# Optimization experiments

Measured on AMD Instinct MI355X. Metric: run time of the kernel, lower is better.

## Reference

```python
import jax, jax.numpy as jnp
import numpy as np

B, T, D, H = 4, 2048, 1024, 16
DH = D // H  # head dim = 64
FLOAT_MIN = jnp.finfo(jnp.float32).min


def setup_inputs() -> dict:
    key = jax.random.key(0)
    k1, k2, k3 = jax.random.split(key, 3)
    scale = 1.0 / np.sqrt(D)
    return {
        "x": jax.random.normal(k1, (B, T, D), dtype=jnp.float32),
        "W_qkv": jax.random.normal(k2, (D, 3 * D), dtype=jnp.float32) * scale,
        "b_qkv": jnp.zeros((3 * D,), dtype=jnp.float32),
        "W_out": jax.random.normal(k3, (D, D), dtype=jnp.float32) * scale,
        "b_out": jnp.zeros((D,), dtype=jnp.float32),
        "mask": jnp.ones((B, T, T), dtype=jnp.float32),
    }


def _split_heads(t):
    # [B, T, D] -> [B, H, T, DH]
    b, s, _ = t.shape
    return t.reshape(b, s, H, DH).transpose(0, 2, 1, 3)


def reference(x, W_qkv, b_qkv, W_out, b_out, mask):
    # fused QKV projection (Conv1D kernel-size 1 == per-position dense)
    qkv = jnp.einsum("btd,de->bte", x, W_qkv) + b_qkv
    q, k, v = jnp.split(qkv, 3, axis=-1)
    q = _split_heads(q) * (DH ** -0.5)  # [B, H, T, DH]
    k = _split_heads(k)
    v = _split_heads(v)
    # scores [B, H, Tq, Tk]
    dot = jnp.einsum("bhqd,bhkd->bhqk", q, k)
    m = mask[:, None, :, :]  # expand over heads
    dot = dot * m + (1.0 - m) * FLOAT_MIN
    attn = jax.nn.softmax(dot, axis=-1)
    ctx = jnp.einsum("bhqk,bhkd->bhqd", attn, v)  # [B, H, T, DH]
    combined = ctx.transpose(0, 2, 1, 3).reshape(x.shape[0], x.shape[1], D)
    out = jnp.einsum("btd,de->bte", combined, W_out) + b_out
    return out
```

## Files before the change

kernel.cpp:

```cpp
#include <hip/hip_runtime.h>

typedef short bf16x8 __attribute__((ext_vector_type(8)));
typedef float f32x4 __attribute__((ext_vector_type(4)));
typedef float f32x16 __attribute__((ext_vector_type(16)));
typedef unsigned short u16x8 __attribute__((ext_vector_type(8)));

#define DEVI __device__ __forceinline__

static constexpr int T_ = 2048;

DEVI unsigned short f2bf(float f) {
  unsigned int x = __builtin_bit_cast(unsigned int, f);
  x += 0x7fffu + ((x >> 16) & 1u);
  return (unsigned short)(x >> 16);
}

DEVI unsigned int cvtpk(float lo, float hi2) {
  unsigned int r;
  asm("v_cvt_pk_bf16_f32 %0, %1, %2" : "=v"(r) : "v"(lo), "v"(hi2));
  return r;
}

DEVI float exp2_raw(float x) {
  float r;
  asm("v_exp_f32 %0, %1" : "=v"(r) : "v"(x));
  return r;
}

DEVI int swz23(int r) {
  const int d = ((r >> 2) ^ (r >> 3)) & 1;
  return r ^ (d << 2) ^ (d << 3);
}

DEVI bf16x8 mkfrag(unsigned a, unsigned b, unsigned c, unsigned d) {
  union { unsigned u[4]; bf16x8 v; } x;
  x.u[0] = a; x.u[1] = b; x.u[2] = c; x.u[3] = d;
  return x.v;
}

DEVI void gl2lds16(const void* g, const void* l) {
  __builtin_amdgcn_global_load_lds(
      (const __attribute__((address_space(1))) void*)g,
      (__attribute__((address_space(3))) void*)l, 16, 0, 0);
}

__global__ __launch_bounds__(256) void k_cvt_bf16(const float* __restrict__ in,
                                                  unsigned short* __restrict__ out) {
  size_t i = ((size_t)blockIdx.x * 256 + threadIdx.x) * 8;
  float4 a = *(const float4*)(in + i);
  float4 b = *(const float4*)(in + i + 4);
  u16x8 o;
  o[0] = f2bf(a.x); o[1] = f2bf(a.y); o[2] = f2bf(a.z); o[3] = f2bf(a.w);
  o[4] = f2bf(b.x); o[5] = f2bf(b.y); o[6] = f2bf(b.z); o[7] = f2bf(b.w);
  *(u16x8*)(out + i) = o;
}

__global__ __launch_bounds__(256) void k_mask_scan(const uint4* __restrict__ m,
                                                   unsigned int* __restrict__ flag) {
  const unsigned int ONE = 0x3f800000u;
  size_t i0 = ((size_t)blockIdx.x * 256 + threadIdx.x) * 8;
  bool ok = true;
#pragma unroll
  for (int i = 0; i < 8; ++i) {
    uint4 v = m[i0 + i];
    ok &= (v.x == ONE) & (v.y == ONE) & (v.z == ONE) & (v.w == ONE);
  }
  if (!ok) atomicAnd(flag, 0u);
}

template <int R, int C>
__global__ __launch_bounds__(256) void k_transpose_cvt(const float* __restrict__ in,
                                                       unsigned short* __restrict__ out) {
  __shared__ unsigned short t[64][65];
  const int c0 = blockIdx.x * 64, r0 = blockIdx.y * 64;
  const int cc = threadIdx.x & 63, r4 = threadIdx.x >> 6;
#pragma unroll
  for (int i = 0; i < 16; ++i) {
    int rr = i * 4 + r4;
    t[rr][cc] = f2bf(in[(size_t)(r0 + rr) * C + c0 + cc]);
  }
  __syncthreads();
#pragma unroll
  for (int i = 0; i < 16; ++i) {
    int rr = i * 4 + r4;
    out[(size_t)(c0 + rr) * R + r0 + cc] = t[cc][rr];
  }
}

__global__ __launch_bounds__(256) void k_transpose_v(const unsigned short* __restrict__ V,
                                                     unsigned short* __restrict__ Vt) {
  __shared__ unsigned short t[64][65];
  const int t0 = blockIdx.x * 64;
  const size_t bh = blockIdx.y;
  const unsigned short* src = V + (bh * T_ + t0) * 64;
  unsigned short* dst = Vt + bh * 64 * T_ + t0;
  const int cc = threadIdx.x & 63, r4 = threadIdx.x >> 6;
#pragma unroll
  for (int i = 0; i < 16; ++i) {
    int rr = i * 4 + r4;
    t[rr][cc] = src[(size_t)rr * 64 + cc];
  }
  __syncthreads();
#pragma unroll
  for (int i = 0; i < 16; ++i) {
    int rr = i * 4 + r4;
    dst[(size_t)rr * T_ + cc] = t[cc][rr];
  }
}

template <int EPI>
__global__ __launch_bounds__(256, 3) void k_gemm(
    const unsigned short* __restrict__ A, const unsigned short* __restrict__ Bt,
    const float* __restrict__ bias,
    unsigned short* __restrict__ qo, unsigned short* __restrict__ ko2,
    unsigned short* __restrict__ vo, float* __restrict__ fo) {
  __shared__ unsigned short As[2][128 * 32];
  __shared__ unsigned short Bs[2][128 * 32];
  const int tid = threadIdx.x;
  const int lane = tid & 63, w = tid >> 6;
  const int wr = w >> 1, wc = w & 1;
  const int g = lane >> 4, c0 = lane & 15;
  const int m0 = blockIdx.y * 128, n0 = blockIdx.x * 128;

  f32x4 acc[4][4] = {};

  const int s0 = tid, s1 = tid + 256;
  const int ar0 = s0 >> 2, ac0 = (s0 & 3) ^ ((ar0 >> 1) & 3);
  const int ar1 = s1 >> 2, ac1 = (s1 & 3) ^ ((ar1 >> 1) & 3);
  const int ldsb0 = w * 512, ldsb1 = w * 512 + 2048;

  const unsigned short* Ar0 = A + (size_t)(m0 + ar0) * 1024 + ac0 * 8;
  const unsigned short* Ar1 = A + (size_t)(m0 + ar1) * 1024 + ac1 * 8;
  const unsigned short* Br0 = Bt + (size_t)(n0 + ar0) * 1024 + ac0 * 8;
  const unsigned short* Br1 = Bt + (size_t)(n0 + ar1) * 1024 + ac1 * 8;

  auto stage = [&](int buf, int kt) {
    const int ke = kt * 32;
    gl2lds16(Ar0 + ke, &As[buf][ldsb0]);
    gl2lds16(Ar1 + ke, &As[buf][ldsb1]);
    gl2lds16(Br0 + ke, &Bs[buf][ldsb0]);
    gl2lds16(Br1 + ke, &Bs[buf][ldsb1]);
  };

  stage(0, 0);
  __syncthreads();
  int cur = 0;
  for (int kt = 0; kt < 32; ++kt) {
    if (kt + 1 < 32) stage(cur ^ 1, kt + 1);
    bf16x8 af[4], bfv[4];
#pragma unroll
    for (int mf = 0; mf < 4; ++mf) {
      int row = wr * 64 + mf * 16 + c0;
      int ch = g ^ ((row >> 1) & 3);
      af[mf] = *(const bf16x8*)&As[cur][row * 32 + ch * 8];
    }
#pragma unroll
    for (int nf = 0; nf < 4; ++nf) {
      int row = wc * 64 + nf * 16 + c0;
      int ch = g ^ ((row >> 1) & 3);
      bfv[nf] = *(const bf16x8*)&Bs[cur][row * 32 + ch * 8];
    }
    __builtin_amdgcn_s_setprio(1);
#pragma unroll
    for (int mf = 0; mf < 4; ++mf)
#pragma unroll
      for (int nf = 0; nf < 4; ++nf)
        acc[mf][nf] = __builtin_amdgcn_mfma_f32_16x16x32_bf16(af[mf], bfv[nf], acc[mf][nf], 0, 0, 0);
    __builtin_amdgcn_s_setprio(0);
    __syncthreads();
    cur ^= 1;
  }

#pragma unroll
  for (int mf = 0; mf < 4; ++mf) {
#pragma unroll
    for (int nf = 0; nf < 4; ++nf) {
      const int n = n0 + wc * 64 + nf * 16 + c0;
      const float bv = bias[n];
#pragma unroll
      for (int r = 0; r < 4; ++r) {
        const int m = m0 + wr * 64 + mf * 16 + g * 4 + r;
        float v = acc[mf][nf][r] + bv;
        if constexpr (EPI == 0) {
          const int sel = n >> 10, hd = n & 1023;
          const int h = hd >> 6, d = hd & 63;
          const int b = m >> 11, t = m & 2047;
          const size_t off = ((size_t)((b * 16 + h) * 2048 + t)) * 64 + d;
          if (sel == 0)       qo[off] = f2bf(v * 0.125f);
          else if (sel == 1)  ko2[off] = f2bf(v);
          else                vo[off] = f2bf(v);
        } else {
          fo[(size_t)m * 1024 + n] = v;
        }
      }
    }
  }
}

__global__ __launch_bounds__(256, 4) void k_attn(
    const unsigned short* __restrict__ Q, const unsigned short* __restrict__ Kg_,
    const unsigned short* __restrict__ Vt, const float* __restrict__ mask,
    const unsigned int* __restrict__ maskflag,
    unsigned short* __restrict__ ctx) {
  __shared__ unsigned short Ks[2][64 * 64];
  __shared__ unsigned short Vs[2][64 * 64];
  const int tid = threadIdx.x, lane = tid & 63, w = tid >> 6;
  const int q = lane & 31, hi = lane >> 5;

  const int flat = blockIdx.x + 16 * blockIdx.y + 256 * blockIdx.z;
  const int work = (flat & 7) * 128 + (flat >> 3);
  const int qb = work & 15;
  const int bh_i = work >> 4;
  const int h = bh_i & 15, b = bh_i >> 4;
  const int t0 = qb * 128;
  const size_t bh = (size_t)bh_i;

  const unsigned short* Qg = Q + (bh * 2048 + t0 + w * 32 + q) * 64;
  const unsigned short* Kg = Kg_ + bh * 2048 * 64;
  const unsigned short* Vg = Vt + bh * 64 * 2048;
  const float* Mg = mask + (size_t)b * 2048 * 2048;
  const bool allones = (*maskflag != 0u);

  bf16x8 qf[4];
#pragma unroll
  for (int kd = 0; kd < 4; ++kd)
    qf[kd] = *(const bf16x8*)(Qg + kd * 16 + hi * 8);

  f32x16 ot[2] = {};
  float mrun = -__builtin_inff(), lrun = 0.f;

  const int s0 = tid, s1 = tid + 256;
  const int kr0 = s0 >> 3, kc0 = (s0 & 7) ^ (kr0 & 7);
  const int kr1 = s1 >> 3, kc1 = (s1 & 7) ^ (kr1 & 7);
  const int kp0 = swz23(kr0), kp1 = swz23(kr1);
  const int ldsb0 = w * 512, ldsb1 = w * 512 + 2048;

  auto stageKV = [&](int buf, int kt) {
    gl2lds16(Kg + (size_t)(kt * 64 + kp0) * 64 + kc0 * 8, &Ks[buf][ldsb0]);
    gl2lds16(Kg + (size_t)(kt * 64 + kp1) * 64 + kc1 * 8, &Ks[buf][ldsb1]);
    gl2lds16(Vg + (size_t)kr0 * 2048 + kt * 64 + kc0 * 8, &Vs[buf][ldsb0]);
    gl2lds16(Vg + (size_t)kr1 * 2048 + kt * 64 + kc1 * 8, &Vs[buf][ldsb1]);
  };

  stageKV(0, 0);
  __syncthreads();
  int cur = 0;
  const float MINF = -3.402823466e38f;
  const float L2E = 1.4426950408889634f;

  for (int kt = 0; kt < 32; ++kt) {
    if (kt + 1 < 32) stageKV(cur ^ 1, kt + 1);

    f32x16 st[2] = {};
#pragma unroll
    for (int mt2 = 0; mt2 < 2; ++mt2) {
      __builtin_amdgcn_s_setprio(1);
#pragma unroll
      for (int kd = 0; kd < 4; ++kd) {
        const int row = mt2 * 32 + q;
        const int ch = (2 * kd + hi) ^ (row & 7);
        bf16x8 kf = *(const bf16x8*)&Ks[cur][row * 64 + ch * 8];
        st[mt2] = __builtin_amdgcn_mfma_f32_32x32x16_bf16(kf, qf[kd], st[mt2], 0, 0, 0);
      }
      __builtin_amdgcn_s_setprio(0);
    }

    if (!allones) {
      const int qg = t0 + w * 32 + q;
#pragma unroll
      for (int mt2 = 0; mt2 < 2; ++mt2)
#pragma unroll
        for (int r = 0; r < 16; ++r) {
          const int kg = kt * 64 + mt2 * 32 +
                         (r & 3) + 4 * ((r >> 2) & 1) + 8 * hi + 16 * (r >> 3);
          const float mv = Mg[(size_t)qg * 2048 + kg];
          st[mt2][r] = st[mt2][r] * mv + (1.f - mv) * MINF;
        }
    }

    float g4[8];
#pragma unroll
    for (int i = 0; i < 4; ++i) {
      g4[i]     = fmaxf(fmaxf(fmaxf(st[0][4 * i], st[0][4 * i + 1]), st[0][4 * i + 2]), st[0][4 * i + 3]);
      g4[i + 4] = fmaxf(fmaxf(fmaxf(st[1][4 * i], st[1][4 * i + 1]), st[1][4 * i + 2]), st[1][4 * i + 3]);
    }
    float r1 = fmaxf(fmaxf(g4[0], g4[1]), g4[2]);
    float r2 = fmaxf(fmaxf(g4[3], g4[4]), g4[5]);
    float r3 = fmaxf(fmaxf(g4[6], g4[7]), r1);
    float tmax = fmaxf(r2, r3);
    tmax = fmaxf(tmax, __shfl_xor(tmax, 32));
    const bool defer = (__all(tmax <= mrun + 8.f) != 0);
    float alpha = 1.f;
    if (!defer) {
      const float mnew = fmaxf(mrun, tmax);
      alpha = exp2_raw((mrun - mnew) * L2E);
      mrun = mnew;
    }
    const float mL2 = mrun * L2E;
#pragma unroll
    for (int mt2 = 0; mt2 < 2; ++mt2)
#pragma unroll
      for (int i = 0; i < 16; ++i)
        st[mt2][i] = exp2_raw(st[mt2][i] * L2E - mL2);
    float s8[8];
#pragma unroll
    for (int i = 0; i < 8; ++i)
      s8[i] = (st[0][i] + st[0][i + 8]) + (st[1][i] + st[1][i + 8]);
    float s4a = s8[0] + s8[4], s4b = s8[1] + s8[5];
    float s4c = s8[2] + s8[6], s4d = s8[3] + s8[7];
    float ps = (s4a + s4b) + (s4c + s4d);
    ps += __shfl_xor(ps, 32);
    lrun = lrun * alpha + ps;
    if (!defer) {
#pragma unroll
      for (int dt = 0; dt < 2; ++dt)
#pragma unroll
        for (int i = 0; i < 16; ++i) ot[dt][i] *= alpha;
    }

    bf16x8 pf[4];
#pragma unroll
    for (int mt2 = 0; mt2 < 2; ++mt2) {
      unsigned int pw[8];
#pragma unroll
      for (int i = 0; i < 8; ++i) pw[i] = cvtpk(st[mt2][2 * i], st[mt2][2 * i + 1]);
      pf[2 * mt2]     = mkfrag(pw[0], pw[1], pw[2], pw[3]);
      pf[2 * mt2 + 1] = mkfrag(pw[4], pw[5], pw[6], pw[7]);
    }

#pragma unroll
    for (int dt = 0; dt < 2; ++dt) {
      __builtin_amdgcn_s_setprio(1);
#pragma unroll
      for (int kt2 = 0; kt2 < 4; ++kt2) {
        const int row = dt * 32 + q;
        const int ch = (2 * kt2 + hi) ^ (row & 7);
        bf16x8 vf = *(const bf16x8*)&Vs[cur][row * 64 + ch * 8];
        ot[dt] = __builtin_amdgcn_mfma_f32_32x32x16_bf16(vf, pf[kt2], ot[dt], 0, 0, 0);
      }
      __builtin_amdgcn_s_setprio(0);
    }

    __syncthreads();
    cur ^= 1;
  }

  const int qg = t0 + w * 32 + q;
  const float rl = 1.f / lrun;
  unsigned short* cp = ctx + ((size_t)b * 2048 + qg) * 1024 + h * 64;
#pragma unroll
  for (int dt = 0; dt < 2; ++dt) {
#pragma unroll
    for (int rg = 0; rg < 4; ++rg) {
      const int d0 = dt * 32 + rg * 8 + hi * 4;
      ushort4 o;
      o.x = f2bf(ot[dt][rg * 4 + 0] * rl);
      o.y = f2bf(ot[dt][rg * 4 + 1] * rl);
      o.z = f2bf(ot[dt][rg * 4 + 2] * rl);
      o.w = f2bf(ot[dt][rg * 4 + 3] * rl);
      *(ushort4*)(cp + d0) = o;
    }
  }
}

extern "C" void kernel_launch(void* const* d_in, const int* in_sizes, int n_in,
                              void* d_out, int out_size, void* d_ws, size_t ws_size,
                              hipStream_t stream) {
  (void)in_sizes; (void)n_in; (void)out_size; (void)ws_size;
  const float* x    = (const float*)d_in[0];
  const float* Wqkv = (const float*)d_in[1];
  const float* bqkv = (const float*)d_in[2];
  const float* Wout = (const float*)d_in[3];
  const float* bout = (const float*)d_in[4];
  const float* mask = (const float*)d_in[5];
  float* out = (float*)d_out;
  char* ws = (char*)d_ws;

  const size_t SZ_BTD = (size_t)8192 * 1024 * 2;
  unsigned short* xb  = (unsigned short*)(ws);
  unsigned short* Wqt = (unsigned short*)(ws + SZ_BTD);
  unsigned short* Wot = (unsigned short*)(ws + SZ_BTD + 6291456);
  unsigned short* Qb  = (unsigned short*)(ws + SZ_BTD + 8388608);
  unsigned short* Kb  = (unsigned short*)(ws + SZ_BTD + 8388608 + SZ_BTD);
  unsigned short* Vb  = (unsigned short*)(ws + SZ_BTD + 8388608 + 2 * SZ_BTD);
  unsigned short* Vtb = (unsigned short*)(ws + SZ_BTD + 8388608 + 3 * SZ_BTD);
  unsigned int* flag  = (unsigned int*)(ws + SZ_BTD + 8388608 + 4 * SZ_BTD);
  unsigned short* ctx = xb;

  hipMemsetAsync(flag, 1, 4, stream);
  k_mask_scan<<<2048, 256, 0, stream>>>((const uint4*)mask, flag);
  k_cvt_bf16<<<4096, 256, 0, stream>>>(x, xb);
  k_transpose_cvt<1024, 3072><<<dim3(48, 16), 256, 0, stream>>>(Wqkv, Wqt);
  k_transpose_cvt<1024, 1024><<<dim3(16, 16), 256, 0, stream>>>(Wout, Wot);
  k_gemm<0><<<dim3(24, 64), 256, 0, stream>>>(xb, Wqt, bqkv, Qb, Kb, Vb, nullptr);
  k_transpose_v<<<dim3(32, 64), 256, 0, stream>>>(Vb, Vtb);
  k_attn<<<dim3(16, 16, 4), 256, 0, stream>>>(Qb, Kb, Vtb, mask, flag, ctx);
  k_gemm<1><<<dim3(8, 64), 256, 0, stream>>>(ctx, Wot, bout, nullptr, nullptr, nullptr, out);
}
```

Before: 230.8 us.

## Use packed f32 math in softmax and retune GEMM occupancy and priority

The attention softmax now uses packed v_pk_fma/v_pk_add/v_pk_mul f32 instructions for the scale-and-shift, the row-sum reduction and the output rescale, roughly halving the VALU instruction count on that path. Separately, the GEMM kernel's launch bounds go from 3 to 2 waves-per-SIMD minimum, and the s_setprio raise around its MFMA loop is removed. The summation order changes slightly, and inline asm may limit compiler scheduling.

```diff
diff --git a/kernel.cpp b/kernel.cpp
--- a/kernel.cpp
+++ b/kernel.cpp
@@ -1,6 +1,7 @@
 #include <hip/hip_runtime.h>
 
 typedef short bf16x8 __attribute__((ext_vector_type(8)));
+typedef float f32x2 __attribute__((ext_vector_type(2)));
 typedef float f32x4 __attribute__((ext_vector_type(4)));
 typedef float f32x16 __attribute__((ext_vector_type(16)));
 typedef unsigned short u16x8 __attribute__((ext_vector_type(8)));
@@ -26,6 +27,25 @@
   asm("v_exp_f32 %0, %1" : "=v"(r) : "v"(x));
   return r;
 }
+
+DEVI f32x2 pk_add(f32x2 a, f32x2 b) {
+  f32x2 r;
+  asm("v_pk_add_f32 %0, %1, %2" : "=v"(r) : "v"(a), "v"(b));
+  return r;
+}
+DEVI f32x2 pk_mul(f32x2 a, f32x2 b) {
+  f32x2 r;
+  asm("v_pk_mul_f32 %0, %1, %2" : "=v"(r) : "v"(a), "v"(b));
+  return r;
+}
+DEVI f32x2 pk_fma(f32x2 a, f32x2 b, f32x2 c) {
+  f32x2 r;
+  asm("v_pk_fma_f32 %0, %1, %2, %3" : "=v"(r) : "v"(a), "v"(b), "v"(c));
+  return r;
+}
+DEVI f32x2 mk2(float a, float b) { f32x2 r; r[0] = a; r[1] = b; return r; }
+
+union Pair16 { f32x16 v; f32x2 p[8]; };
 
 DEVI int swz23(int r) {
   const int d = ((r >> 2) ^ (r >> 3)) & 1;
@@ -109,7 +129,7 @@
 }
 
 template <int EPI>
-__global__ __launch_bounds__(256, 3) void k_gemm(
+__global__ __launch_bounds__(256, 2) void k_gemm(
     const unsigned short* __restrict__ A, const unsigned short* __restrict__ Bt,
     const float* __restrict__ bias,
     unsigned short* __restrict__ qo, unsigned short* __restrict__ ko2,
@@ -160,13 +180,11 @@
       int ch = g ^ ((row >> 1) & 3);
       bfv[nf] = *(const bf16x8*)&Bs[cur][row * 32 + ch * 8];
     }
-    __builtin_amdgcn_s_setprio(1);
 #pragma unroll
     for (int mf = 0; mf < 4; ++mf)
 #pragma unroll
       for (int nf = 0; nf < 4; ++nf)
         acc[mf][nf] = __builtin_amdgcn_mfma_f32_16x16x32_bf16(af[mf], bfv[nf], acc[mf][nf], 0, 0, 0);
-    __builtin_amdgcn_s_setprio(0);
     __syncthreads();
     cur ^= 1;
   }
@@ -297,35 +315,52 @@
       mrun = mnew;
     }
     const float mL2 = mrun * L2E;
-#pragma unroll
-    for (int mt2 = 0; mt2 < 2; ++mt2)
-#pragma unroll
-      for (int i = 0; i < 16; ++i)
-        st[mt2][i] = exp2_raw(st[mt2][i] * L2E - mL2);
-    float s8[8];
-#pragma unroll
-    for (int i = 0; i < 8; ++i)
-      s8[i] = (st[0][i] + st[0][i + 8]) + (st[1][i] + st[1][i + 8]);
-    float s4a = s8[0] + s8[4], s4b = s8[1] + s8[5];
-    float s4c = s8[2] + s8[6], s4d = s8[3] + s8[7];
-    float ps = (s4a + s4b) + (s4c + s4d);
+
+    Pair16 a0, a1; a0.v = st[0]; a1.v = st[1];
+    const f32x2 cL2 = mk2(L2E, L2E);
+    const f32x2 cm  = mk2(-mL2, -mL2);
+#pragma unroll
+    for (int i = 0; i < 8; ++i) {
+      a0.p[i] = pk_fma(a0.p[i], cL2, cm);
+      a1.p[i] = pk_fma(a1.p[i], cL2, cm);
+    }
+#pragma unroll
+    for (int i = 0; i < 16; ++i) {
+      a0.v[i] = exp2_raw(a0.v[i]);
+      a1.v[i] = exp2_raw(a1.v[i]);
+    }
+    f32x2 t2[8];
+#pragma unroll
+    for (int i = 0; i < 8; ++i) t2[i] = pk_add(a0.p[i], a1.p[i]);
+    f32x2 u0 = pk_add(t2[0], t2[4]), u1 = pk_add(t2[1], t2[5]);
+    f32x2 u2 = pk_add(t2[2], t2[6]), u3 = pk_add(t2[3], t2[7]);
+    f32x2 vv0 = pk_add(u0, u1), vv1 = pk_add(u2, u3);
+    f32x2 wv = pk_add(vv0, vv1);
+    float ps = wv[0] + wv[1];
     ps += __shfl_xor(ps, 32);
     lrun = lrun * alpha + ps;
     if (!defer) {
-#pragma unroll
-      for (int dt = 0; dt < 2; ++dt)
-#pragma unroll
-        for (int i = 0; i < 16; ++i) ot[dt][i] *= alpha;
+      const f32x2 al2 = mk2(alpha, alpha);
+#pragma unroll
+      for (int dt = 0; dt < 2; ++dt) {
+        Pair16 o; o.v = ot[dt];
+#pragma unroll
+        for (int i = 0; i < 8; ++i) o.p[i] = pk_mul(o.p[i], al2);
+        ot[dt] = o.v;
+      }
     }
 
     bf16x8 pf[4];
-#pragma unroll
-    for (int mt2 = 0; mt2 < 2; ++mt2) {
+    {
       unsigned int pw[8];
 #pragma unroll
-      for (int i = 0; i < 8; ++i) pw[i] = cvtpk(st[mt2][2 * i], st[mt2][2 * i + 1]);
-      pf[2 * mt2]     = mkfrag(pw[0], pw[1], pw[2], pw[3]);
-      pf[2 * mt2 + 1] = mkfrag(pw[4], pw[5], pw[6], pw[7]);
+      for (int i = 0; i < 8; ++i) pw[i] = cvtpk(a0.v[2 * i], a0.v[2 * i + 1]);
+      pf[0] = mkfrag(pw[0], pw[1], pw[2], pw[3]);
+      pf[1] = mkfrag(pw[4], pw[5], pw[6], pw[7]);
+#pragma unroll
+      for (int i = 0; i < 8; ++i) pw[i] = cvtpk(a1.v[2 * i], a1.v[2 * i + 1]);
+      pf[2] = mkfrag(pw[0], pw[1], pw[2], pw[3]);
+      pf[3] = mkfrag(pw[4], pw[5], pw[6], pw[7]);
     }
 
 #pragma unroll
```

Result: no change. 231.4 us (+0.3%).
